# Optimization experiments

Measured on AMD Instinct MI355X. Metric: run time of the kernel, lower is better.

Reference implementation:

```python
import jax, jax.numpy as jnp
import numpy as np

C_FINE, C_MID, C_COARSE = 100, 20, 5
EPS = 1e-12


def setup_inputs() -> dict:
    key = jax.random.key(0)
    k1, k2 = jax.random.split(key)
    N, D = 262144, 128
    representations = jax.random.normal(k1, (N, D), dtype=jnp.float32)
    target_fine = jax.random.randint(k2, (N,), 0, C_FINE, dtype=jnp.int32)
    # nested hierarchy: fine -> mid (5 fines per mid), fine -> coarse (20 fines per coarse)
    fine2mid = (jnp.arange(C_FINE, dtype=jnp.int32) // (C_FINE // C_MID)).astype(jnp.int32)
    fine2coarse = (jnp.arange(C_FINE, dtype=jnp.int32) // (C_FINE // C_COARSE)).astype(jnp.int32)
    return {
        "representations": representations,
        "target_fine": target_fine,
        "fine2mid": fine2mid,
        "fine2coarse": fine2coarse,
    }


def _safe_norm(diff):
    # L2 norm along last axis; eps gives a 0 subgradient at diff==0
    return jnp.sqrt(jnp.sum(diff * diff, axis=-1) + EPS)


def _segment_mean(x, ids, num_segments):
    ones = jnp.ones(x.shape[:1], x.dtype)
    s = jax.ops.segment_sum(x, ids, num_segments=num_segments)
    c = jax.ops.segment_sum(ones, ids, num_segments=num_segments)
    return s / jnp.maximum(c, 1.0)[:, None]


def reference(representations, target_fine, fine2mid, fine2coarse):
    # ---- tree construction (vectorized version of the per-class Python loops) ----
    # fine prototypes: mean of representations per fine class  [C_FINE, D]
    fine_protos = _segment_mean(representations, target_fine, C_FINE)
    # mid prototypes: mean of child fine prototypes  [C_MID, D]
    mid_protos = _segment_mean(fine_protos, fine2mid, C_MID)
    # coarse prototypes: mean of child mid prototypes  [C_COARSE, D]
    mid2coarse = jax.ops.segment_max(fine2coarse, fine2mid, num_segments=C_MID)
    coarse_protos = _segment_mean(mid_protos, mid2coarse, C_COARSE)
    # (the root node contributes ||root - root|| = 0 to every pair, so it is omitted)

    # ---- pairwise tree-path distances over all fine-class pairs ----
    iu, ju = np.triu_indices(C_FINE, k=1)  # static C*(C-1)/2 = 4950 pairs
    ci, cj = fine2coarse[iu], fine2coarse[ju]
    mi, mj = fine2mid[iu], fine2mid[ju]
    tree_d = _safe_norm(coarse_protos[ci] - coarse_protos[cj]) \
           + _safe_norm(mid_protos[mi] - mid_protos[mj])
    # Euclidean distances between fine prototypes
    proto_d = _safe_norm(fine_protos[iu] - fine_protos[ju])

    # ---- CPCC: loss = 1 - Pearson correlation(tree_d, proto_d) ----
    tc = tree_d - jnp.mean(tree_d)
    pc = proto_d - jnp.mean(proto_d)
    corr = jnp.sum(tc * pc) / jnp.sqrt(jnp.sum(tc * tc) * jnp.sum(pc * pc) + EPS)
    return 1.0 - corr
```

## Files before the change

### kernel.cpp

```cpp
#include <hip/hip_runtime.h>
#include <math.h>

#define C_FINE   100
#define C_MID    20
#define C_COARSE 5
#define D        128
#define NROWS    262144
#define NPAIRS   4950
#define NBLK4    78

#define WPG      768
#define BATCH    16
#define NBATCH   (NROWS/BATCH)
#define RG       8
#define RB       (WPG/RG)
#define PSTR     12928

#define FP_OFF    0
#define DM_OFF    12800
#define DC_OFF    13200
#define ACC_OFF   13232
#define DONE_OFF  13244
#define CNT_OFF   13248
#define FSUM_OFF  13360
#define PART_OFF  26176

__global__ __launch_bounds__(64) void kAcc(const float* __restrict__ rep,
                                           const int* __restrict__ tgt,
                                           float* __restrict__ ws) {
    __shared__ float acc[C_FINE][D];
    __shared__ float cnt[C_FINE];
    const int lane = threadIdx.x;
    const int wid  = blockIdx.x;

    for (int e = lane; e < C_FINE * D / 4; e += 64)
        ((float4*)acc)[e] = make_float4(0.f, 0.f, 0.f, 0.f);
    for (int e = lane; e < C_FINE; e += 64) cnt[e] = 0.f;
    if (wid == 0) {
        for (int e = lane; e < 3228; e += 64)
            ((float4*)(ws + CNT_OFF))[e] = make_float4(0.f, 0.f, 0.f, 0.f);
    }
    __syncthreads();

    const float4* rep4 = (const float4*)rep;
    const int2*   tgt2 = (const int2*)tgt;

    for (int b = wid; b < NBATCH; b += WPG) {
        const int base = b * BATCH;
        float4 v[8]; int2 cc[8];
        #pragma unroll
        for (int u = 0; u < 8; ++u)
            v[u] = rep4[(size_t)(base + 2 * u) * 32 + lane];
        #pragma unroll
        for (int u = 0; u < 8; ++u)
            cc[u] = tgt2[base / 2 + u];
        #pragma unroll
        for (int u = 0; u < 8; ++u) {
            const int cA = cc[u].x, cB = cc[u].y;
            if (cA == cB) {
                float4 w;
                w.x = __shfl(v[u].x, lane | 32);
                w.y = __shfl(v[u].y, lane | 32);
                w.z = __shfl(v[u].z, lane | 32);
                w.w = __shfl(v[u].w, lane | 32);
                if (lane < 32) {
                    float4 a = *(float4*)&acc[cA][lane * 4];
                    a.x += v[u].x + w.x; a.y += v[u].y + w.y;
                    a.z += v[u].z + w.z; a.w += v[u].w + w.w;
                    *(float4*)&acc[cA][lane * 4] = a;
                    if (lane == 0) cnt[cA] += 2.f;
                }
            } else {
                const int myc = (lane < 32) ? cA : cB;
                const int dl  = (lane & 31) * 4;
                float4 a = *(float4*)&acc[myc][dl];
                a.x += v[u].x; a.y += v[u].y; a.z += v[u].z; a.w += v[u].w;
                *(float4*)&acc[myc][dl] = a;
                if ((lane & 31) == 0) cnt[myc] += 1.f;
            }
        }
    }
    __syncthreads();

    float* part = ws + PART_OFF + (size_t)wid * PSTR;
    for (int e = lane; e < C_FINE * D / 4; e += 64)
        ((float4*)part)[e] = ((const float4*)acc)[e];
    for (int e = lane; e < C_FINE; e += 64) part[12800 + e] = cnt[e];
}

__global__ __launch_bounds__(128) void kRed(float* __restrict__ ws) {
    const int c = blockIdx.x >> 3, g = blockIdx.x & 7;
    const int t = threadIdx.x;
    const float* p = ws + PART_OFF + (size_t)(g * RB) * PSTR + c * D + t;
    float s = 0.f;
    #pragma unroll 8
    for (int b = 0; b < RB; ++b) s += p[(size_t)b * PSTR];
    atomicAdd(ws + FSUM_OFF + c * D + t, s);

    float cl = (t < RB) ? ws[PART_OFF + (size_t)(g * RB + t) * PSTR + 12800 + c] : 0.f;
    for (int off = 32; off > 0; off >>= 1) cl += __shfl_down(cl, off);
    __shared__ float r2[2];
    if ((t & 63) == 0) r2[t >> 6] = cl;
    __syncthreads();
    if (t == 0) atomicAdd(ws + CNT_OFF + c, r2[0] + r2[1]);
}

__global__ __launch_bounds__(256) void k3_hier(const int* __restrict__ f2m,
                                               const int* __restrict__ f2c,
                                               float* __restrict__ ws) {
    __shared__ float fineP[C_FINE][D];
    __shared__ float midP[C_MID][D + 1];
    __shared__ float coarP[C_COARSE][D + 1];
    __shared__ int   sf2m[C_FINE], sf2c[C_FINE], m2c[C_MID];
    __shared__ float midCnt[C_MID], coarCnt[C_COARSE];
    __shared__ float sTot[C_FINE];
    const int t = threadIdx.x;

    if (t < C_FINE) {
        sf2m[t] = f2m[t]; sf2c[t] = f2c[t];
        sTot[t] = ws[CNT_OFF + t];
    }
    for (int e = t; e < C_MID * (D + 1); e += 256) ((float*)midP)[e] = 0.f;
    for (int e = t; e < C_COARSE * (D + 1); e += 256) ((float*)coarP)[e] = 0.f;
    __syncthreads();

    for (int e = t; e < C_FINE * D; e += 256) {
        int c = e >> 7, d = e & 127;
        float v = ws[FSUM_OFF + e] / fmaxf(sTot[c], 1.f);
        fineP[c][d] = v;
        ws[FP_OFF + e] = v;
    }
    if (t < C_MID) {
        int cntv = 0, mx = -2147483647;
        for (int f = 0; f < C_FINE; ++f)
            if (sf2m[f] == t) { ++cntv; mx = max(mx, sf2c[f]); }
        midCnt[t] = (float)max(cntv, 1);
        m2c[t] = mx;
    }
    __syncthreads();

    if (t < D) {
        const int d = t;
        for (int f = 0; f < C_FINE; ++f)
            midP[sf2m[f]][d] += fineP[f][d];
        for (int m = 0; m < C_MID; ++m)
            midP[m][d] /= midCnt[m];
    }
    if (t >= 128 && t < 128 + C_COARSE) {
        int cc = t - 128, cntv = 0;
        for (int m = 0; m < C_MID; ++m) if (m2c[m] == cc) ++cntv;
        coarCnt[cc] = (float)max(cntv, 1);
    }
    __syncthreads();

    if (t < D) {
        const int d = t;
        for (int m = 0; m < C_MID; ++m)
            coarP[m2c[m]][d] += midP[m][d];
        for (int cc = 0; cc < C_COARSE; ++cc)
            coarP[cc][d] /= coarCnt[cc];
    }
    __syncthreads();

    for (int e = t; e < C_MID * C_MID; e += 256) {
        int m1 = e / C_MID, m2 = e % C_MID;
        float ss = 0.f;
        #pragma unroll 8
        for (int d = 0; d < D; ++d) {
            float df = midP[m1][d] - midP[m2][d];
            ss += df * df;
        }
        ws[DM_OFF + e] = sqrtf(ss + 1e-12f);
    }
    for (int e = t; e < C_COARSE * C_COARSE; e += 256) {
        int c1 = e / C_COARSE, c2 = e % C_COARSE;
        float ss = 0.f;
        #pragma unroll 8
        for (int d = 0; d < D; ++d) {
            float df = coarP[c1][d] - coarP[c2][d];
            ss += df * df;
        }
        ws[DC_OFF + e] = sqrtf(ss + 1e-12f);
    }
    if (t < 5) ((double*)(ws + ACC_OFF))[t] = 0.0;
    if (t == 5) ((int*)ws + DONE_OFF)[0] = 0;
}

__global__ __launch_bounds__(64) void k45_pairs(float* __restrict__ ws,
                                                const int* __restrict__ f2m,
                                                const int* __restrict__ f2c,
                                                float* __restrict__ out) {
    const int p = blockIdx.x * 64 + threadIdx.x;
    double st = 0, sp = 0, stp = 0, stt = 0, spp = 0;
    if (p < NPAIRS) {
        int i = 0, rem = p;
        while (rem >= C_FINE - 1 - i) { rem -= C_FINE - 1 - i; ++i; }
        int j = i + 1 + rem;

        const float4* Fi = (const float4*)(ws + FP_OFF + i * D);
        const float4* Fj = (const float4*)(ws + FP_OFF + j * D);
        float ss = 0.f;
        #pragma unroll
        for (int k = 0; k < D / 4; ++k) {
            float4 a = Fi[k], b = Fj[k];
            float dx = a.x - b.x, dy = a.y - b.y, dz = a.z - b.z, dw = a.w - b.w;
            ss += dx * dx + dy * dy + dz * dz + dw * dw;
        }
        float proto = sqrtf(ss + 1e-12f);
        float tree  = ws[DC_OFF + f2c[i] * C_COARSE + f2c[j]]
                    + ws[DM_OFF + f2m[i] * C_MID + f2m[j]];
        st = tree; sp = proto;
        stp = (double)tree * (double)proto;
        stt = (double)tree * (double)tree;
        spp = (double)proto * (double)proto;
    }
    for (int off = 32; off > 0; off >>= 1) {
        st  += __shfl_down(st, off);
        sp  += __shfl_down(sp, off);
        stp += __shfl_down(stp, off);
        stt += __shfl_down(stt, off);
        spp += __shfl_down(spp, off);
    }
    if (threadIdx.x == 0) {
        double* acc = (double*)(ws + ACC_OFF);
        atomicAdd(&acc[0], st);
        atomicAdd(&acc[1], sp);
        atomicAdd(&acc[2], stp);
        atomicAdd(&acc[3], stt);
        atomicAdd(&acc[4], spp);
        __threadfence();
        int* done = (int*)ws + DONE_OFF;
        int ticket = atomicAdd(done, 1);
        if (ticket == NBLK4 - 1) {
            double fst  = atomicAdd(&acc[0], 0.0);
            double fsp  = atomicAdd(&acc[1], 0.0);
            double fstp = atomicAdd(&acc[2], 0.0);
            double fstt = atomicAdd(&acc[3], 0.0);
            double fspp = atomicAdd(&acc[4], 0.0);
            const double n = (double)NPAIRS;
            double num = fstp - fst * fsp / n;
            double dtt = fstt - fst * fst / n;
            double dpp = fspp - fsp * fsp / n;
            double corr = num / sqrt(dtt * dpp + 1e-12);
            out[0] = (float)(1.0 - corr);
        }
    }
}

extern "C" void kernel_launch(void* const* d_in, const int* in_sizes, int n_in,
                              void* d_out, int out_size, void* d_ws, size_t ws_size,
                              hipStream_t stream) {
    const float* rep = (const float*)d_in[0];
    const int*   tgt = (const int*)d_in[1];
    const int*   f2m = (const int*)d_in[2];
    const int*   f2c = (const int*)d_in[3];
    float* ws  = (float*)d_ws;
    float* out = (float*)d_out;

    hipLaunchKernelGGL(kAcc,      dim3(WPG),         dim3(64),  0, stream, rep, tgt, ws);
    hipLaunchKernelGGL(kRed,      dim3(C_FINE * RG), dim3(128), 0, stream, ws);
    hipLaunchKernelGGL(k3_hier,   dim3(1),           dim3(256), 0, stream, f2m, f2c, ws);
    hipLaunchKernelGGL(k45_pairs, dim3(NBLK4),       dim3(64),  0, stream,
                       ws, f2m, f2c, out);
}
```

Measured before the change: 91.51 us.

## Widen accumulation blocks to four waves with per-dimension split and prefetching

The segment-sum accumulation kernel moves from one 64-thread wave per block to four waves. Each wave owns a 32-dimension slice, and each half-wave owns one row of a pair, so the same-class branch and shuffles go away. The next batch of rows and targets is loaded into registers before the current batch is accumulated into shared memory, so global loads overlap the LDS updates. The trade-off is scalar 4-byte loads in place of float4, an LDS atomic for each count update, and more threads sharing a single 51KB shared accumulator per block.

```diff
diff --git a/kernel.cpp b/kernel.cpp
--- a/kernel.cpp
+++ b/kernel.cpp
@@ -25,67 +25,77 @@
 #define FSUM_OFF  13360
 #define PART_OFF  26176
 
-__global__ __launch_bounds__(64) void kAcc(const float* __restrict__ rep,
-                                           const int* __restrict__ tgt,
-                                           float* __restrict__ ws) {
+__global__ __launch_bounds__(256) void kAcc(const float* __restrict__ rep,
+                                            const int* __restrict__ tgt,
+                                            float* __restrict__ ws) {
     __shared__ float acc[C_FINE][D];
     __shared__ float cnt[C_FINE];
-    const int lane = threadIdx.x;
+    const int t    = threadIdx.x;
+    const int w    = t >> 6;
+    const int lane = t & 63;
+    const int half = lane >> 5;
+    const int dl   = lane & 31;
     const int wid  = blockIdx.x;
-
-    for (int e = lane; e < C_FINE * D / 4; e += 64)
+    const int dimoff = 32 * w + dl;
+
+    for (int e = t; e < C_FINE * D / 4; e += 256)
         ((float4*)acc)[e] = make_float4(0.f, 0.f, 0.f, 0.f);
-    for (int e = lane; e < C_FINE; e += 64) cnt[e] = 0.f;
+    if (t < C_FINE) cnt[t] = 0.f;
     if (wid == 0) {
-        for (int e = lane; e < 3228; e += 64)
+        for (int e = t; e < 3228; e += 256)
             ((float4*)(ws + CNT_OFF))[e] = make_float4(0.f, 0.f, 0.f, 0.f);
     }
     __syncthreads();
 
-    const float4* rep4 = (const float4*)rep;
-    const int2*   tgt2 = (const int2*)tgt;
-
-    for (int b = wid; b < NBATCH; b += WPG) {
-        const int base = b * BATCH;
-        float4 v[8]; int2 cc[8];
-        #pragma unroll
-        for (int u = 0; u < 8; ++u)
-            v[u] = rep4[(size_t)(base + 2 * u) * 32 + lane];
-        #pragma unroll
-        for (int u = 0; u < 8; ++u)
-            cc[u] = tgt2[base / 2 + u];
+    const int2* tgt2 = (const int2*)tgt;
+
+    float v[8]; int2 cc[8];
+    int g = wid;
+    {
+        const int base = g * BATCH;
         #pragma unroll
         for (int u = 0; u < 8; ++u) {
-            const int cA = cc[u].x, cB = cc[u].y;
-            if (cA == cB) {
-                float4 w;
-                w.x = __shfl(v[u].x, lane | 32);
-                w.y = __shfl(v[u].y, lane | 32);
-                w.z = __shfl(v[u].z, lane | 32);
-                w.w = __shfl(v[u].w, lane | 32);
-                if (lane < 32) {
-                    float4 a = *(float4*)&acc[cA][lane * 4];
-                    a.x += v[u].x + w.x; a.y += v[u].y + w.y;
-                    a.z += v[u].z + w.z; a.w += v[u].w + w.w;
-                    *(float4*)&acc[cA][lane * 4] = a;
-                    if (lane == 0) cnt[cA] += 2.f;
-                }
-            } else {
-                const int myc = (lane < 32) ? cA : cB;
-                const int dl  = (lane & 31) * 4;
-                float4 a = *(float4*)&acc[myc][dl];
-                a.x += v[u].x; a.y += v[u].y; a.z += v[u].z; a.w += v[u].w;
-                *(float4*)&acc[myc][dl] = a;
-                if ((lane & 31) == 0) cnt[myc] += 1.f;
+            cc[u] = tgt2[base / 2 + u];
+            v[u]  = rep[(size_t)(base + 2 * u + half) * D + dimoff];
+        }
+    }
+    for (;;) {
+        const int gn = g + WPG;
+        if (gn < NBATCH) {
+            float vn[8]; int2 ccn[8];
+            const int base = gn * BATCH;
+            #pragma unroll
+            for (int u = 0; u < 8; ++u) {
+                ccn[u] = tgt2[base / 2 + u];
+                vn[u]  = rep[(size_t)(base + 2 * u + half) * D + dimoff];
             }
+            #pragma unroll
+            for (int u = 0; u < 8; ++u) {
+                const int c = half ? cc[u].y : cc[u].x;
+                acc[c][dimoff] += v[u];
+                if (w == 0 && dl == 0)
+                    atomicAdd(&cnt[c], 1.f);
+            }
+            #pragma unroll
+            for (int u = 0; u < 8; ++u) { v[u] = vn[u]; cc[u] = ccn[u]; }
+            g = gn;
+        } else {
+            #pragma unroll
+            for (int u = 0; u < 8; ++u) {
+                const int c = half ? cc[u].y : cc[u].x;
+                acc[c][dimoff] += v[u];
+                if (w == 0 && dl == 0)
+                    atomicAdd(&cnt[c], 1.f);
+            }
+            break;
         }
     }
     __syncthreads();
 
     float* part = ws + PART_OFF + (size_t)wid * PSTR;
-    for (int e = lane; e < C_FINE * D / 4; e += 64)
+    for (int e = t; e < C_FINE * D / 4; e += 256)
         ((float4*)part)[e] = ((const float4*)acc)[e];
-    for (int e = lane; e < C_FINE; e += 64) part[12800 + e] = cnt[e];
+    if (t < C_FINE) part[12800 + t] = cnt[t];
 }
 
 __global__ __launch_bounds__(128) void kRed(float* __restrict__ ws) {
@@ -257,7 +267,7 @@
     float* ws  = (float*)d_ws;
     float* out = (float*)d_out;
 
-    hipLaunchKernelGGL(kAcc,      dim3(WPG),         dim3(64),  0, stream, rep, tgt, ws);
+    hipLaunchKernelGGL(kAcc,      dim3(WPG),         dim3(256), 0, stream, rep, tgt, ws);
     hipLaunchKernelGGL(kRed,      dim3(C_FINE * RG), dim3(128), 0, stream, ws);
     hipLaunchKernelGGL(k3_hier,   dim3(1),           dim3(256), 0, stream, f2m, f2c, ws);
     hipLaunchKernelGGL(k45_pairs, dim3(NBLK4),       dim3(64),  0, stream,
```

Result: slower. 124.3 us (+35.8%).

## Compute per-class segment sums with bf16 MFMA one-hot matmuls

Applied to the files above, without the earlier changes.

Replaces the LDS scatter-accumulate segment sum with a one-hot matrix multiply on MFMA units. Representations are rounded to bf16 and multiplied by a one-hot class matrix, accumulating 112x128 partials per block, while counts come from a shared-memory histogram. The reduction kernel becomes one block per class with no atomics. This trades exact fp32 sums for bf16-rounded inputs, a precision risk, to remove LDS read-modify-write bottlenecks and branch divergence.

```diff
diff --git a/kernel.cpp b/kernel.cpp
--- a/kernel.cpp
+++ b/kernel.cpp
@@ -9,12 +9,11 @@
 #define NPAIRS   4950
 #define NBLK4    78
 
-#define WPG      768
-#define BATCH    16
-#define NBATCH   (NROWS/BATCH)
-#define RG       8
-#define RB       (WPG/RG)
-#define PSTR     12928
+#define NB       512
+#define ROWS_PB  (NROWS/NB)
+#define NSTEP    (ROWS_PB/32)
+#define MT       7
+#define PSTR2    (113*128)
 
 #define FP_OFF    0
 #define DM_OFF    12800
@@ -22,87 +21,126 @@
 #define ACC_OFF   13232
 #define DONE_OFF  13244
 #define CNT_OFF   13248
-#define FSUM_OFF  13360
+#define FSUM_OFF  13376
 #define PART_OFF  26176
 
-__global__ __launch_bounds__(64) void kAcc(const float* __restrict__ rep,
+typedef __attribute__((ext_vector_type(8))) short bf16x8;
+typedef __attribute__((ext_vector_type(4))) float f32x4;
+
+static __device__ __forceinline__ unsigned short f2bf(float f) {
+    unsigned int x = __float_as_uint(f);
+    x += 0x7FFF + ((x >> 16) & 1);
+    return (unsigned short)(x >> 16);
+}
+
+__global__ __launch_bounds__(256) void kMF(const float* __restrict__ rep,
                                            const int* __restrict__ tgt,
                                            float* __restrict__ ws) {
-    __shared__ float acc[C_FINE][D];
-    __shared__ float cnt[C_FINE];
-    const int lane = threadIdx.x;
-    const int wid  = blockIdx.x;
-
-    for (int e = lane; e < C_FINE * D / 4; e += 64)
-        ((float4*)acc)[e] = make_float4(0.f, 0.f, 0.f, 0.f);
-    for (int e = lane; e < C_FINE; e += 64) cnt[e] = 0.f;
-    if (wid == 0) {
-        for (int e = lane; e < 3228; e += 64)
-            ((float4*)(ws + CNT_OFF))[e] = make_float4(0.f, 0.f, 0.f, 0.f);
-    }
-    __syncthreads();
-
-    const float4* rep4 = (const float4*)rep;
-    const int2*   tgt2 = (const int2*)tgt;
-
-    for (int b = wid; b < NBATCH; b += WPG) {
-        const int base = b * BATCH;
-        float4 v[8]; int2 cc[8];
+    __shared__ int hist[128];
+    const int t  = threadIdx.x;
+    const int w  = t >> 6;
+    const int l  = t & 63;
+    const int lg = l >> 4;
+    const int ll = l & 15;
+    const int blk   = blockIdx.x;
+    const int rbase = blk * ROWS_PB;
+
+    if (t < 128) hist[t] = 0;
+    __syncthreads();
+    atomicAdd(&hist[tgt[rbase + t]], 1);
+    atomicAdd(&hist[tgt[rbase + t + 256]], 1);
+
+    const int colbase = 32 * w + ll;
+
+    f32x4 acc[MT][2];
+    #pragma unroll
+    for (int m = 0; m < MT; ++m)
         #pragma unroll
-        for (int u = 0; u < 8; ++u)
-            v[u] = rep4[(size_t)(base + 2 * u) * 32 + lane];
+        for (int n = 0; n < 2; ++n)
+            #pragma unroll
+            for (int i = 0; i < 4; ++i) acc[m][n][i] = 0.f;
+
+    float vA[16], vB[16];
+    int   tA[8],  tB[8];
+
+#define LOADSTEP(V, T, s) do {                                                  \
+    const float* p_ = rep + ((size_t)(rbase + (s) * 32 + 8 * lg) * D + colbase);\
+    _Pragma("unroll")                                                           \
+    for (int j_ = 0; j_ < 8; ++j_) {                                            \
+        V[j_]     = p_[j_ * D];                                                 \
+        V[8 + j_] = p_[j_ * D + 16];                                            \
+    }                                                                           \
+    const int* q_ = tgt + (rbase + (s) * 32 + 8 * lg);                          \
+    _Pragma("unroll")                                                           \
+    for (int j_ = 0; j_ < 8; ++j_) T[j_] = q_[j_];                              \
+} while (0)
+
+#define COMPSTEP(V, T) do {                                                     \
+    bf16x8 b0_, b1_;                                                            \
+    _Pragma("unroll")                                                           \
+    for (int j_ = 0; j_ < 8; ++j_) {                                            \
+        b0_[j_] = (short)f2bf(V[j_]);                                           \
+        b1_[j_] = (short)f2bf(V[8 + j_]);                                       \
+    }                                                                           \
+    _Pragma("unroll")                                                           \
+    for (int m_ = 0; m_ < MT; ++m_) {                                           \
+        const int cb_ = 16 * m_ + ll;                                           \
+        bf16x8 a_;                                                              \
+        _Pragma("unroll")                                                       \
+        for (int j_ = 0; j_ < 8; ++j_)                                          \
+            a_[j_] = (T[j_] == cb_) ? (short)0x3F80 : (short)0;                 \
+        acc[m_][0] = __builtin_amdgcn_mfma_f32_16x16x32_bf16(a_, b0_, acc[m_][0], 0, 0, 0); \
+        acc[m_][1] = __builtin_amdgcn_mfma_f32_16x16x32_bf16(a_, b1_, acc[m_][1], 0, 0, 0); \
+    }                                                                           \
+} while (0)
+
+    LOADSTEP(vA, tA, 0);
+    #pragma unroll 1
+    for (int s = 0; s < NSTEP; s += 2) {
+        LOADSTEP(vB, tB, s + 1);
+        COMPSTEP(vA, tA);
+        if (s + 2 < NSTEP) LOADSTEP(vA, tA, s + 2);
+        COMPSTEP(vB, tB);
+    }
+#undef LOADSTEP
+#undef COMPSTEP
+
+    float* part = ws + PART_OFF + (size_t)blk * PSTR2;
+    #pragma unroll
+    for (int m = 0; m < MT; ++m)
         #pragma unroll
-        for (int u = 0; u < 8; ++u)
-            cc[u] = tgt2[base / 2 + u];
-        #pragma unroll
-        for (int u = 0; u < 8; ++u) {
-            const int cA = cc[u].x, cB = cc[u].y;
-            if (cA == cB) {
-                float4 w;
-                w.x = __shfl(v[u].x, lane | 32);
-                w.y = __shfl(v[u].y, lane | 32);
-                w.z = __shfl(v[u].z, lane | 32);
-                w.w = __shfl(v[u].w, lane | 32);
-                if (lane < 32) {
-                    float4 a = *(float4*)&acc[cA][lane * 4];
-                    a.x += v[u].x + w.x; a.y += v[u].y + w.y;
-                    a.z += v[u].z + w.z; a.w += v[u].w + w.w;
-                    *(float4*)&acc[cA][lane * 4] = a;
-                    if (lane == 0) cnt[cA] += 2.f;
-                }
-            } else {
-                const int myc = (lane < 32) ? cA : cB;
-                const int dl  = (lane & 31) * 4;
-                float4 a = *(float4*)&acc[myc][dl];
-                a.x += v[u].x; a.y += v[u].y; a.z += v[u].z; a.w += v[u].w;
-                *(float4*)&acc[myc][dl] = a;
-                if ((lane & 31) == 0) cnt[myc] += 1.f;
-            }
-        }
-    }
-    __syncthreads();
-
-    float* part = ws + PART_OFF + (size_t)wid * PSTR;
-    for (int e = lane; e < C_FINE * D / 4; e += 64)
-        ((float4*)part)[e] = ((const float4*)acc)[e];
-    for (int e = lane; e < C_FINE; e += 64) part[12800 + e] = cnt[e];
-}
-
-__global__ __launch_bounds__(128) void kRed(float* __restrict__ ws) {
-    const int c = blockIdx.x >> 3, g = blockIdx.x & 7;
+        for (int n = 0; n < 2; ++n)
+            #pragma unroll
+            for (int i = 0; i < 4; ++i)
+                part[(16 * m + 4 * lg + i) * D + 32 * w + 16 * n + ll] = acc[m][n][i];
+    __syncthreads();
+    if (t < 128) part[112 * D + t] = (t < C_FINE) ? (float)hist[t] : 0.f;
+}
+
+__global__ __launch_bounds__(512) void kRed(float* __restrict__ ws) {
+    const int c = blockIdx.x;
     const int t = threadIdx.x;
-    const float* p = ws + PART_OFF + (size_t)(g * RB) * PSTR + c * D + t;
+    const int g = t >> 7, d = t & 127;
     float s = 0.f;
     #pragma unroll 8
-    for (int b = 0; b < RB; ++b) s += p[(size_t)b * PSTR];
-    atomicAdd(ws + FSUM_OFF + c * D + t, s);
-
-    float cl = (t < RB) ? ws[PART_OFF + (size_t)(g * RB + t) * PSTR + 12800 + c] : 0.f;
-    for (int off = 32; off > 0; off >>= 1) cl += __shfl_down(cl, off);
-    __shared__ float r2[2];
-    if ((t & 63) == 0) r2[t >> 6] = cl;
-    __syncthreads();
-    if (t == 0) atomicAdd(ws + CNT_OFF + c, r2[0] + r2[1]);
+    for (int b = g; b < NB; b += 4)
+        s += ws[PART_OFF + (size_t)b * PSTR2 + c * D + d];
+    __shared__ float red[4][128];
+    red[g][d] = s;
+
+    float cv = ws[PART_OFF + (size_t)t * PSTR2 + 112 * D + c];
+    #pragma unroll
+    for (int off = 32; off > 0; off >>= 1) cv += __shfl_down(cv, off);
+    __shared__ float cw[8];
+    if ((t & 63) == 0) cw[t >> 6] = cv;
+    __syncthreads();
+    if (g == 0) ws[FSUM_OFF + c * D + d] = red[0][d] + red[1][d] + red[2][d] + red[3][d];
+    if (t == 0) {
+        float tot = 0.f;
+        #pragma unroll
+        for (int q = 0; q < 8; ++q) tot += cw[q];
+        ws[CNT_OFF + c] = tot;
+    }
 }
 
 __global__ __launch_bounds__(256) void k3_hier(const int* __restrict__ f2m,
@@ -257,9 +295,9 @@
     float* ws  = (float*)d_ws;
     float* out = (float*)d_out;
 
-    hipLaunchKernelGGL(kAcc,      dim3(WPG),         dim3(64),  0, stream, rep, tgt, ws);
-    hipLaunchKernelGGL(kRed,      dim3(C_FINE * RG), dim3(128), 0, stream, ws);
-    hipLaunchKernelGGL(k3_hier,   dim3(1),           dim3(256), 0, stream, f2m, f2c, ws);
-    hipLaunchKernelGGL(k45_pairs, dim3(NBLK4),       dim3(64),  0, stream,
+    hipLaunchKernelGGL(kMF,       dim3(NB),     dim3(256), 0, stream, rep, tgt, ws);
+    hipLaunchKernelGGL(kRed,      dim3(C_FINE), dim3(512), 0, stream, ws);
+    hipLaunchKernelGGL(k3_hier,   dim3(1),      dim3(256), 0, stream, f2m, f2c, ws);
+    hipLaunchKernelGGL(k45_pairs, dim3(NBLK4),  dim3(64),  0, stream,
                        ws, f2m, f2c, out);
 }
```

Result: faster. 81.99 us (-10.4%).
